# Performance work log

Measured on AMD Instinct MI355X. Metric: run time of the kernel, lower is better.

## Reference

```python
import jax, jax.numpy as jnp
import numpy as np

MAX_CONTEXT = 100
NUM_HEADS = 4
GRU_GROUPS = 4


def _layernorm(x, g, b, eps=1e-5):
    m = jnp.mean(x, axis=-1, keepdims=True)
    v = jnp.mean((x - m) ** 2, axis=-1, keepdims=True)
    return (x - m) / jnp.sqrt(v + eps) * g + b


def _grouped_gru(x, wih, whh, bih, bhh, G):
    # x: [N, T, C]; shared GRU params run on each channel group (PyTorch gate order r,z,n)
    N, T, C = x.shape
    D = C // G
    xg = x.reshape(N, T, G, D)
    xp = jnp.einsum('ntgd,ed->ntge', xg, wih) + bih  # e = 3D, precomputed input projections
    xp = jnp.moveaxis(xp, 1, 0)  # [T, N, G, 3D]

    def step(h, xt):
        gh = jnp.einsum('ngd,ed->nge', h, whh) + bhh
        xr, xz, xn = jnp.split(xt, 3, axis=-1)
        hr, hz, hn = jnp.split(gh, 3, axis=-1)
        r = jax.nn.sigmoid(xr + hr)
        z = jax.nn.sigmoid(xz + hz)
        n = jnp.tanh(xn + r * hn)
        h = (1.0 - z) * n + z * h
        return h, h

    h0 = jnp.zeros((N, G, D), x.dtype)
    _, hs = jax.lax.scan(step, h0, xp)  # hs: [T, N, G, D]
    return jnp.moveaxis(hs, 0, 1).reshape(N, T, C)


def _mha(x, wqkv, bqkv, wo, bo, H, max_ctx):
    # batch_first self-attention with causal + truncated-window additive mask
    N, T, C = x.shape
    Dh = C // H
    qkv = x @ wqkv.T + bqkv
    q, k, v = jnp.split(qkv, 3, axis=-1)
    q = q.reshape(N, T, H, Dh)
    k = k.reshape(N, T, H, Dh)
    v = v.reshape(N, T, H, Dh)
    scale = 1.0 / np.sqrt(Dh).astype(np.float32)
    scores = jnp.einsum('nqhd,nkhd->nhqk', q, k) * scale
    i = jnp.arange(T)
    diff = i[:, None] - i[None, :]
    allowed = (diff >= 0) & (diff <= max_ctx)
    scores = jnp.where(allowed, scores, -jnp.inf)
    attn = jax.nn.softmax(scores, axis=-1)
    out = jnp.einsum('nhqk,nkhd->nqhd', attn, v).reshape(N, T, C)
    return out @ wo.T + bo


def setup_inputs() -> dict:
    key = jax.random.key(0)
    ks = jax.random.split(key, 5)
    B, C, T, F = 2, 128, 512, 64
    D = C // GRU_GROUPS
    s = 0.1
    return {
        'x': jax.random.normal(ks[0], (B, C, T, F), jnp.float32),
        'ln1_g': jnp.ones((C,), jnp.float32),
        'ln1_b': jnp.zeros((C,), jnp.float32),
        'gru_wih': jax.random.normal(ks[1], (3 * D, D), jnp.float32) * s,
        'gru_whh': jax.random.normal(ks[2], (3 * D, D), jnp.float32) * s,
        'gru_bih': jnp.zeros((3 * D,), jnp.float32),
        'gru_bhh': jnp.zeros((3 * D,), jnp.float32),
        'ln2_g': jnp.ones((C,), jnp.float32),
        'ln2_b': jnp.zeros((C,), jnp.float32),
        'in_proj_w': jax.random.normal(ks[3], (3 * C, C), jnp.float32) * s,
        'in_proj_b': jnp.zeros((3 * C,), jnp.float32),
        'out_proj_w': jax.random.normal(ks[4], (C, C), jnp.float32) * s,
        'out_proj_b': jnp.zeros((C,), jnp.float32),
    }


def reference(x, ln1_g, ln1_b, gru_wih, gru_whh, gru_bih, gru_bhh, ln2_g, ln2_b, in_proj_w, in_proj_b, out_proj_w, out_proj_b):
    B, C, T, F = x.shape
    # [B, C, T, F] -> [B*F, T, C]: each freq bin is an independent time sequence
    seq = jnp.transpose(x, (0, 3, 2, 1)).reshape(B * F, T, C)
    seq = seq + _grouped_gru(_layernorm(seq, ln1_g, ln1_b), gru_wih, gru_whh, gru_bih, gru_bhh, GRU_GROUPS)
    seq = seq + _mha(_layernorm(seq, ln2_g, ln2_b), in_proj_w, in_proj_b, out_proj_w, out_proj_b, NUM_HEADS, MAX_CONTEXT)
    return jnp.transpose(seq.reshape(B, F, T, C), (0, 3, 2, 1))
```

## Files before the change

kernel.cpp:

```cpp
#include <hip/hip_runtime.h>
#include <hip/hip_bf16.h>
#include <math.h>


typedef __attribute__((ext_vector_type(8))) short short8;
typedef __attribute__((ext_vector_type(4))) float f32x4;
typedef __attribute__((ext_vector_type(2))) float f32x2;

__device__ __forceinline__ float bflo(unsigned int u) { return __uint_as_float(u << 16); }
__device__ __forceinline__ float bfhi(unsigned int u) { return __uint_as_float(u & 0xffff0000u); }
__device__ __forceinline__ float bf2f(unsigned short u) { return __uint_as_float(((unsigned int)u) << 16); }
__device__ __forceinline__ unsigned short f2bf(float f) {
  __hip_bfloat16 h = __float2bfloat16(f);
  return *reinterpret_cast<unsigned short*>(&h);
}

typedef __attribute__((address_space(1))) const unsigned int uint_g;
typedef __attribute__((address_space(3))) unsigned int uint_l;
__device__ __forceinline__ void glds16(const void* g, void* l) {
  __builtin_amdgcn_global_load_lds((uint_g*)g, (uint_l*)l, 16, 0, 0);
}

__global__ __launch_bounds__(256) void transpose_in_ln_kernel(const float* __restrict__ x,
                                                              float* __restrict__ seq,
                                                              const float* __restrict__ gam,
                                                              const float* __restrict__ bet,
                                                              unsigned short* __restrict__ out,
                                                              const float* __restrict__ wih,
                                                              unsigned short* __restrict__ wih_b,
                                                              const float* __restrict__ inw,
                                                              unsigned short* __restrict__ inw_b,
                                                              const float* __restrict__ outw,
                                                              unsigned short* __restrict__ outw_b) {
  {
    int g_ = blockIdx.x * 256 + threadIdx.x;
    if (g_ < 3072) wih_b[g_] = f2bf(wih[g_]);
    else if (g_ < 52224) inw_b[g_ - 3072] = f2bf(inw[g_ - 3072]);
    else if (g_ < 68608) outw_b[g_ - 52224] = f2bf(outw[g_ - 52224]);
  }

  __shared__ float tile[128 * 65];
  int b = blockIdx.x >> 9;
  int t = blockIdx.x & 511;
  for (int i = threadIdx.x; i < 128 * 64; i += 256) {
    int c = i >> 6, f = i & 63;
    tile[c * 65 + f] = x[(((size_t)(b * 128 + c)) * 512 + t) * 64 + f];
  }
  __syncthreads();
  for (int i = threadIdx.x; i < 64 * 128; i += 256) {
    int f = i >> 7, c = i & 127;
    seq[(((size_t)(b * 64 + f)) * 512 + t) * 128 + c] = tile[c * 65 + f];
  }

  const int f = threadIdx.x >> 2, q = threadIdx.x & 3;
  float s = 0.f, ss = 0.f;
  #pragma unroll
  for (int u = 0; u < 32; ++u) {
    float v = tile[(q * 32 + u) * 65 + f];
    s += v; ss += v * v;
  }
  s += __shfl_xor(s, 1); s += __shfl_xor(s, 2);
  ss += __shfl_xor(ss, 1); ss += __shfl_xor(ss, 2);
  float mean = s * (1.f / 128.f);
  float var = ss * (1.f / 128.f) - mean * mean;
  float rs = rsqrtf(var + 1e-5f);

  unsigned int* orow = (unsigned int*)(out + (((size_t)(b * 64 + f)) * 512 + t) * 128);
  #pragma unroll
  for (int u = 0; u < 8; ++u) {
    int c0 = q * 32 + u * 4;
    float4 gg = ((const float4*)gam)[c0 >> 2];
    float4 bb = ((const float4*)bet)[c0 >> 2];
    float v0 = tile[(c0 + 0) * 65 + f], v1 = tile[(c0 + 1) * 65 + f];
    float v2 = tile[(c0 + 2) * 65 + f], v3 = tile[(c0 + 3) * 65 + f];
    float o0 = (v0 - mean) * rs * gg.x + bb.x;
    float o1 = (v1 - mean) * rs * gg.y + bb.y;
    float o2 = (v2 - mean) * rs * gg.z + bb.z;
    float o3 = (v3 - mean) * rs * gg.w + bb.w;
    orow[(c0 >> 1) + 0] = ((unsigned int)f2bf(o1) << 16) | (unsigned int)f2bf(o0);
    orow[(c0 >> 1) + 1] = ((unsigned int)f2bf(o3) << 16) | (unsigned int)f2bf(o2);
  }
}

__global__ __launch_bounds__(256) void transpose_out_kernel(const float* __restrict__ seq, float* __restrict__ out) {
  __shared__ float tile[128 * 65];
  int b = blockIdx.x >> 9;
  int t = blockIdx.x & 511;
  for (int i = threadIdx.x; i < 64 * 128; i += 256) {
    int f = i >> 7, c = i & 127;
    tile[c * 65 + f] = seq[(((size_t)(b * 64 + f)) * 512 + t) * 128 + c];
  }
  __syncthreads();
  for (int i = threadIdx.x; i < 128 * 64; i += 256) {
    int c = i >> 6, f = i & 63;
    out[(((size_t)(b * 128 + c)) * 512 + t) * 64 + f] = tile[c * 65 + f];
  }
}

__global__ __launch_bounds__(256) void ln_kernel(const float* __restrict__ in, const float* __restrict__ g,
                                                 const float* __restrict__ b, unsigned short* __restrict__ out) {
  int row = blockIdx.x * 4 + (threadIdx.x >> 6);
  int lane = threadIdx.x & 63;
  float2 v = ((const float2*)(in + (size_t)row * 128))[lane];
  float s = v.x + v.y, ss = v.x * v.x + v.y * v.y;
  #pragma unroll
  for (int off = 32; off > 0; off >>= 1) {
    s += __shfl_xor(s, off);
    ss += __shfl_xor(ss, off);
  }
  float mean = s * (1.f / 128.f);
  float var = ss * (1.f / 128.f) - mean * mean;
  float rs = rsqrtf(var + 1e-5f);
  float2 gg = ((const float2*)g)[lane];
  float2 bb = ((const float2*)b)[lane];
  float o0 = (v.x - mean) * rs * gg.x + bb.x;
  float o1 = (v.y - mean) * rs * gg.y + bb.y;
  unsigned int packed = ((unsigned int)f2bf(o1) << 16) | (unsigned int)f2bf(o0);
  ((unsigned int*)(out + (size_t)row * 128))[lane] = packed;
}

template <int K, int MODE>
__global__ __launch_bounds__(256) void gemm_mfma(const unsigned short* __restrict__ A,
                                                 const unsigned short* __restrict__ W,
                                                 const float* __restrict__ bias,
                                                 unsigned short* __restrict__ outB,
                                                 float* __restrict__ outF, int Ncols) {
  const int tid = threadIdx.x;
  const int wave = tid >> 6, lane = tid & 63;
  const int wy = wave >> 1, wx = wave & 1;
  const int lr = lane & 15, lq = lane >> 4;
  const int m0 = blockIdx.x * 128 + wy * 64;
  const int n0 = blockIdx.y * 128 + wx * 64;

  f32x4 acc[4][4];
  #pragma unroll
  for (int i = 0; i < 4; ++i)
    #pragma unroll
    for (int j = 0; j < 4; ++j) acc[i][j] = f32x4{0.f, 0.f, 0.f, 0.f};

  const short8 zfrag = short8{0, 0, 0, 0, 0, 0, 0, 0};

  #pragma unroll
  for (int kk = 0; kk < K; kk += 32) {
    short8 af[4], bfq[4];
    #pragma unroll
    for (int i = 0; i < 4; ++i)
      af[i] = *(const short8*)(A + (size_t)(m0 + i * 16 + lr) * K + kk + lq * 8);
    #pragma unroll
    for (int j = 0; j < 4; ++j) {
      int wr = n0 + j * 16 + lr;
      bfq[j] = (wr < Ncols) ? *(const short8*)(W + (size_t)wr * K + kk + lq * 8) : zfrag;
    }
    #pragma unroll
    for (int i = 0; i < 4; ++i)
      #pragma unroll
      for (int j = 0; j < 4; ++j)
        acc[i][j] = __builtin_amdgcn_mfma_f32_16x16x32_bf16(af[i], bfq[j], acc[i][j], 0, 0, 0);
  }

  #pragma unroll
  for (int j = 0; j < 4; ++j) {
    int col = n0 + j * 16 + lr;
    if (col < Ncols) {
      float bb = bias[col];
      #pragma unroll
      for (int i = 0; i < 4; ++i) {
        #pragma unroll
        for (int r = 0; r < 4; ++r) {
          int row = m0 + i * 16 + lq * 4 + r;
          float v = acc[i][j][r] + bb;
          if (MODE == 0)
            outB[(size_t)row * Ncols + col] = f2bf(v);
          else
            outF[(size_t)row * 128 + col] += v;
        }
      }
    }
  }
}

__global__ __launch_bounds__(64, 1) void gru_kernel(const unsigned short* __restrict__ xp,
                                                    const float* __restrict__ whh,
                                                    const float* __restrict__ bhh,
                                                    float* __restrict__ seq) {
  const int l = threadIdx.x;
  const int half = l >> 5, d = l & 31;
  const int blk = blockIdx.x;
  const int chain = blk * 2 + half;
  const int n = chain >> 2;
  const int g0 = (blk * 2) & 3;

  const float LOG2E = 1.4426950408889634f;
  const float T2LOG2E = 2.8853900817779268f;

  __shared__ __align__(16) unsigned char stage[2][6144];
  __shared__ __align__(16) float h_lds[2][64];
  h_lds[0][l] = 0.f;

  f32x2 wr2[16], wz2[16], wn2[16];
  #pragma unroll
  for (int u = 0; u < 16; ++u) {
    float2 a = *(const float2*)(whh + (size_t)d * 32 + u * 2);
    float2 b = *(const float2*)(whh + (size_t)(32 + d) * 32 + u * 2);
    float2 c = *(const float2*)(whh + (size_t)(64 + d) * 32 + u * 2);
    wr2[u] = f32x2{a.x * LOG2E, a.y * LOG2E};
    wz2[u] = f32x2{b.x * LOG2E, b.y * LOG2E};
    wn2[u] = f32x2{c.x * T2LOG2E, c.y * T2LOG2E};
  }
  #pragma unroll
  for (int u = 0; u < 16; ++u)
    asm volatile("" : "+v"(wr2[u]), "+v"(wz2[u]), "+v"(wn2[u]));

  float br = bhh[d] * LOG2E, bz = bhh[32 + d] * LOG2E, bn = bhh[64 + d] * T2LOG2E;
  asm volatile("" : "+v"(br), "+v"(bz), "+v"(bn));

  const char* xg = (const char*)xp;
  const size_t cb0 = ((size_t)n * 2048 + g0) * 192;
  const size_t cb1 = ((size_t)n * 2048 + g0 + 1) * 192;
  const int fa = l * 16;
  const int oxa = (fa / 192) * 768 + (fa % 192);
  const int fb = 1024 + l * 16;
  const int oxb = (fb / 192) * 768 + (fb % 192);
  const char* px0a = xg + cb0 + oxa;
  const char* px0b = xg + cb0 + oxb;
  const char* px1a = xg + cb1 + oxa;
  const char* px1b = xg + cb1 + oxb;
  const int osa = (l >> 4) * 512 + (l & 15) * 16;
  const size_t sqb0 = ((size_t)n * 512 * 128 + (size_t)g0 * 32) * 4;
  const char* psa = (const char*)seq + sqb0 + osa;
  const char* psb = psa + 2048;

  float* sb = seq + (size_t)n * 512 * 128 + g0 * 32 + l;

  glds16(px0a, stage[0] + 0);
  glds16(px0b, stage[0] + 1024);
  glds16(px1a, stage[0] + 2048);
  glds16(px1b, stage[0] + 3072);
  glds16(psa,  stage[0] + 4096);
  glds16(psb,  stage[0] + 5120);

  float hprev = 0.f;

  for (int c = 0; c < 64; ++c) {
    const int cur = c & 1;
    if (c < 63) {
      const size_t xo = (size_t)(c + 1) * 6144;
      const size_t so = (size_t)(c + 1) * 4096;
      unsigned char* nb = stage[cur ^ 1];
      glds16(px0a + xo, nb + 0);
      glds16(px0b + xo, nb + 1024);
      glds16(px1a + xo, nb + 2048);
      glds16(px1b + xo, nb + 3072);
      glds16(psa + so,  nb + 4096);
      glds16(psb + so,  nb + 5120);
    }
    __builtin_amdgcn_sched_barrier(0);
    if (c == 0)       asm volatile("s_waitcnt vmcnt(6)" ::: "memory");
    else if (c == 63) asm volatile("s_waitcnt vmcnt(8)" ::: "memory");
    else              asm volatile("s_waitcnt vmcnt(14)" ::: "memory");
    __builtin_amdgcn_sched_barrier(0);

    const unsigned char* scur = stage[cur];
    #pragma unroll
    for (int p = 0; p < 8; ++p) {
      const int t = c * 8 + p;

      const f32x4* hsrc = (const f32x4*)&h_lds[p & 1][half * 32];
      f32x2 ar0 = f32x2{br, 0.f}, ar1 = f32x2{0.f, 0.f};
      f32x2 az0 = f32x2{bz, 0.f}, az1 = f32x2{0.f, 0.f};
      f32x2 an0 = f32x2{bn, 0.f}, an1 = f32x2{0.f, 0.f};
      #pragma unroll
      for (int u = 0; u < 8; ++u) {
        f32x4 h4 = hsrc[u];
        f32x2 hlo = f32x2{h4.x, h4.y};
        f32x2 hhi = f32x2{h4.z, h4.w};
        ar0 += wr2[2 * u] * hlo; ar1 += wr2[2 * u + 1] * hhi;
        az0 += wz2[2 * u] * hlo; az1 += wz2[2 * u + 1] * hhi;
        an0 += wn2[2 * u] * hlo; an1 += wn2[2 * u + 1] * hhi;
      }
      f32x2 arv = ar0 + ar1, azv = az0 + az1, anv = an0 + an1;
      float accr = arv.x + arv.y;
      float accz = azv.x + azv.y;
      float accn = anv.x + anv.y;

      const unsigned short* xrow = (const unsigned short*)(scur + half * 2048 + p * 192);
      float xr = bf2f(xrow[d]) * LOG2E;
      float xz = bf2f(xrow[32 + d]) * LOG2E;
      float xn2 = bf2f(xrow[64 + d]) * T2LOG2E;
      float sv0 = *(const float*)(scur + 4096 + p * 256 + (l << 2));

      float r = __builtin_amdgcn_rcpf(1.f + __builtin_amdgcn_exp2f(-(xr + accr)));
      float z = __builtin_amdgcn_rcpf(1.f + __builtin_amdgcn_exp2f(-(xz + accz)));
      float e2 = __builtin_amdgcn_exp2f(xn2 + r * accn);
      float nn = 1.f - 2.f * __builtin_amdgcn_rcpf(e2 + 1.f);
      float hnew = z * (hprev - nn) + nn;
      hprev = hnew;

      h_lds[(p + 1) & 1][l] = hnew;
      sb[(size_t)t * 128] = sv0 + hnew;
    }
  }
}

__global__ __launch_bounds__(256) void attn_oproj_kernel(const unsigned short* __restrict__ qkv,
                                                         const unsigned short* __restrict__ outw_b,
                                                         const float* __restrict__ outb,
                                                         float* __restrict__ seq) {
  const int qbase = blockIdx.x * 64;
  const int n = blockIdx.y;
  const int tid = threadIdx.x;
  const int w = tid >> 6, lane = tid & 63;
  const int lr = lane & 15, lq = lane >> 4;
  const int ws0 = max(0, qbase - 100);

  const int KROWS = 192;
  const int VPITCH = 200;
  const int PPITCH = 40;
  const int OPITCH = 132;

  __shared__ unsigned short KL[192 * 32];
  __shared__ unsigned short VT[32 * 200];
  __shared__ unsigned short PL[4][16 * 40];
  __shared__ float LL[64];
  __shared__ unsigned short OT[64 * 132];

  const char* qkvb = (const char*)qkv;
  const size_t rowb = ((size_t)(n * 512 + ws0)) * 768;
  const int wq0 = qbase + w * 16;

  const float SCL2 = 0.17677669529663687f * 1.4426950408889634f;
  const int lo = max(0, wq0 - 100) - ws0;
  const int hi = wq0 + 15 - ws0;
  const int kc0 = lo >> 5, kc1 = hi >> 5;
  unsigned short* plw = PL[w];

  for (int h = 0; h < 4; ++h) {
    if (h) __syncthreads();

    #pragma unroll
    for (int it = 0; it < 3; ++it) {
      int c = w * 192 + it * 64 + lane;
      const char* src = qkvb + rowb + (size_t)(c >> 2) * 768 + 256 + h * 64 + (size_t)(c & 3) * 16;
      glds16(src, (char*)KL + w * 3072 + it * 1024);
    }
    if (tid < KROWS) {
      const unsigned int* vsrc = (const unsigned int*)(qkvb + rowb + (size_t)tid * 768 + 512 + h * 64);
      #pragma unroll
      for (int u = 0; u < 16; ++u) {
        unsigned int vv = vsrc[u];
        VT[(2 * u) * VPITCH + tid] = (unsigned short)(vv & 0xffff);
        VT[(2 * u + 1) * VPITCH + tid] = (unsigned short)(vv >> 16);
      }
    }
    short8 qfrag = *(const short8*)(qkvb + ((size_t)(n * 512 + wq0 + lr)) * 768 + h * 64 + lq * 16);
    __syncthreads();

    f32x4 oacc0 = f32x4{0.f, 0.f, 0.f, 0.f};
    f32x4 oacc1 = f32x4{0.f, 0.f, 0.f, 0.f};
    float lsum[4] = {0.f, 0.f, 0.f, 0.f};

    for (int kc = kc0; kc <= kc1; ++kc) {
      #pragma unroll
      for (int sub = 0; sub < 2; ++sub) {
        const int kt = kc * 2 + sub;
        short8 kfrag = *(const short8*)(KL + (kt * 16 + lr) * 32 + lq * 8);
        f32x4 s4 = __builtin_amdgcn_mfma_f32_16x16x32_bf16(qfrag, kfrag,
                                                           f32x4{0.f, 0.f, 0.f, 0.f}, 0, 0, 0);
        const int tk = ws0 + kt * 16 + lr;
        #pragma unroll
        for (int r = 0; r < 4; ++r) {
          const int tq = wq0 + lq * 4 + r;
          bool ok = (tk <= tq) && (tk + 100 >= tq);
          float p = ok ? __builtin_amdgcn_exp2f(s4[r] * SCL2) : 0.f;
          lsum[r] += p;
          plw[(lq * 4 + r) * PPITCH + sub * 16 + lr] = f2bf(p);
        }
      }
      short8 pfrag = *(const short8*)(plw + lr * PPITCH + lq * 8);
      short8 vf0 = *(const short8*)(VT + lr * VPITCH + kc * 32 + lq * 8);
      short8 vf1 = *(const short8*)(VT + (16 + lr) * VPITCH + kc * 32 + lq * 8);
      oacc0 = __builtin_amdgcn_mfma_f32_16x16x32_bf16(vf0, pfrag, oacc0, 0, 0, 0);
      oacc1 = __builtin_amdgcn_mfma_f32_16x16x32_bf16(vf1, pfrag, oacc1, 0, 0, 0);
    }

    #pragma unroll
    for (int r = 0; r < 4; ++r) {
      float v = lsum[r];
      v += __shfl_xor(v, 1); v += __shfl_xor(v, 2);
      v += __shfl_xor(v, 4); v += __shfl_xor(v, 8);
      lsum[r] = v;
    }
    if (lr == 0) {
      #pragma unroll
      for (int r = 0; r < 4; ++r) LL[w * 16 + lq * 4 + r] = lsum[r];
    }
    float rl = __builtin_amdgcn_rcpf(LL[w * 16 + lr]);

    {
      unsigned short* orow = OT + (w * 16 + lr) * OPITCH + h * 32 + lq * 4;
      uint2 pk0;
      pk0.x = ((unsigned int)f2bf(oacc0[1] * rl) << 16) | f2bf(oacc0[0] * rl);
      pk0.y = ((unsigned int)f2bf(oacc0[3] * rl) << 16) | f2bf(oacc0[2] * rl);
      *(uint2*)orow = pk0;
      uint2 pk1;
      pk1.x = ((unsigned int)f2bf(oacc1[1] * rl) << 16) | f2bf(oacc1[0] * rl);
      pk1.y = ((unsigned int)f2bf(oacc1[3] * rl) << 16) | f2bf(oacc1[2] * rl);
      *(uint2*)(orow + 16) = pk1;
    }
  }

  __syncthreads();

  f32x4 acc[8];
  #pragma unroll
  for (int j = 0; j < 8; ++j) acc[j] = f32x4{0.f, 0.f, 0.f, 0.f};
  #pragma unroll
  for (int kk = 0; kk < 4; ++kk) {
    short8 af = *(const short8*)(OT + (w * 16 + lr) * OPITCH + kk * 32 + lq * 8);
    #pragma unroll
    for (int j = 0; j < 8; ++j) {
      short8 wf = *(const short8*)(outw_b + (size_t)(j * 16 + lr) * 128 + kk * 32 + lq * 8);
      acc[j] = __builtin_amdgcn_mfma_f32_16x16x32_bf16(af, wf, acc[j], 0, 0, 0);
    }
  }
  #pragma unroll
  for (int j = 0; j < 8; ++j) {
    int col = j * 16 + lr;
    float bb = outb[col];
    #pragma unroll
    for (int r = 0; r < 4; ++r) {
      size_t row = (size_t)n * 512 + qbase + w * 16 + lq * 4 + r;
      seq[row * 128 + col] += acc[j][r] + bb;
    }
  }
}

extern "C" void kernel_launch(void* const* d_in, const int* in_sizes, int n_in,
                              void* d_out, int out_size, void* d_ws, size_t ws_size,
                              hipStream_t stream) {
  const float* x      = (const float*)d_in[0];
  const float* ln1_g  = (const float*)d_in[1];
  const float* ln1_b  = (const float*)d_in[2];
  const float* wih    = (const float*)d_in[3];
  const float* whh    = (const float*)d_in[4];
  const float* bih    = (const float*)d_in[5];
  const float* bhh    = (const float*)d_in[6];
  const float* ln2_g  = (const float*)d_in[7];
  const float* ln2_b  = (const float*)d_in[8];
  const float* inw    = (const float*)d_in[9];
  const float* inb    = (const float*)d_in[10];
  const float* outw   = (const float*)d_in[11];
  const float* outb   = (const float*)d_in[12];

  char* ws = (char*)d_ws;
  float*          seq   = (float*)ws;
  unsigned short* tmpb  = (unsigned short*)(ws + 33554432);
  unsigned short* big   = (unsigned short*)(ws + 50331648);
  unsigned short* wih_b = (unsigned short*)(ws + 100663296);
  unsigned short* inw_b = wih_b + 3072;
  unsigned short* outw_b = inw_b + 49152;

  transpose_in_ln_kernel<<<1024, 256, 0, stream>>>(x, seq, ln1_g, ln1_b, tmpb,
                                                   wih, wih_b, inw, inw_b, outw, outw_b);

  gemm_mfma<32, 0><<<dim3(2048, 1), 256, 0, stream>>>(tmpb, wih_b, bih, big, nullptr, 96);

  gru_kernel<<<256, 64, 0, stream>>>(big, whh, bhh, seq);

  ln_kernel<<<16384, 256, 0, stream>>>(seq, ln2_g, ln2_b, tmpb);

  gemm_mfma<128, 0><<<dim3(512, 3), 256, 0, stream>>>(tmpb, inw_b, inb, big, nullptr, 384);

  attn_oproj_kernel<<<dim3(8, 128), 256, 0, stream>>>(big, outw_b, outb, seq);

  transpose_out_kernel<<<1024, 256, 0, stream>>>(seq, (float*)d_out);
}
```

Baseline: 382.9 us.

## Split attention per head across blocks and fuse output projection into transpose-out

The attention kernel now launches one block per (query tile, head, sequence) rather than looping over four heads inside a block, which gives four times as many blocks and lighter per-block work. It writes the bf16 attention output to a scratch buffer. The output projection and residual add move into the final transpose kernel, which computes them with MFMA and adds them to the LDS tile before the transposed store, removing a separate read-modify-write of seq. In exchange, the attention output makes an extra global round trip, and each head's block reloads its own K/V slices.

```diff
diff --git a/kernel.cpp b/kernel.cpp
--- a/kernel.cpp
+++ b/kernel.cpp
@@ -82,16 +82,51 @@
   }
 }
 
-__global__ __launch_bounds__(256) void transpose_out_kernel(const float* __restrict__ seq, float* __restrict__ out) {
+__global__ __launch_bounds__(256) void transpose_out_oproj_kernel(const float* __restrict__ seq,
+                                                                  const unsigned short* __restrict__ attn,
+                                                                  const unsigned short* __restrict__ outw_b,
+                                                                  const float* __restrict__ outb,
+                                                                  float* __restrict__ out) {
   __shared__ float tile[128 * 65];
   int b = blockIdx.x >> 9;
   int t = blockIdx.x & 511;
-  for (int i = threadIdx.x; i < 64 * 128; i += 256) {
+  const int tid = threadIdx.x;
+  const int w = tid >> 6, lane = tid & 63;
+  const int lr = lane & 15, lq = lane >> 4;
+
+  for (int i = tid; i < 64 * 128; i += 256) {
     int f = i >> 7, c = i & 127;
     tile[c * 65 + f] = seq[(((size_t)(b * 64 + f)) * 512 + t) * 128 + c];
   }
+
+  f32x4 acc[8];
+  #pragma unroll
+  for (int j = 0; j < 8; ++j) acc[j] = f32x4{0.f, 0.f, 0.f, 0.f};
+  const unsigned short* arow = attn + (((size_t)(b * 64 + w * 16 + lr)) * 512 + t) * 128;
+  #pragma unroll
+  for (int kk = 0; kk < 4; ++kk) {
+    short8 af = *(const short8*)(arow + kk * 32 + lq * 8);
+    #pragma unroll
+    for (int j = 0; j < 8; ++j) {
+      short8 wf = *(const short8*)(outw_b + (size_t)(j * 16 + lr) * 128 + kk * 32 + lq * 8);
+      acc[j] = __builtin_amdgcn_mfma_f32_16x16x32_bf16(af, wf, acc[j], 0, 0, 0);
+    }
+  }
   __syncthreads();
-  for (int i = threadIdx.x; i < 128 * 64; i += 256) {
+
+  #pragma unroll
+  for (int j = 0; j < 8; ++j) {
+    int col = j * 16 + lr;
+    float bb = outb[col];
+    #pragma unroll
+    for (int r = 0; r < 4; ++r) {
+      int f = w * 16 + lq * 4 + r;
+      tile[col * 65 + f] += acc[j][r] + bb;
+    }
+  }
+  __syncthreads();
+
+  for (int i = tid; i < 128 * 64; i += 256) {
     int c = i >> 6, f = i & 63;
     out[(((size_t)(b * 128 + c)) * 512 + t) * 64 + f] = tile[c * 65 + f];
   }
@@ -302,12 +337,11 @@
   }
 }
 
-__global__ __launch_bounds__(256) void attn_oproj_kernel(const unsigned short* __restrict__ qkv,
-                                                         const unsigned short* __restrict__ outw_b,
-                                                         const float* __restrict__ outb,
-                                                         float* __restrict__ seq) {
+__global__ __launch_bounds__(256) void attn_kernel(const unsigned short* __restrict__ qkv,
+                                                   unsigned short* __restrict__ outp) {
   const int qbase = blockIdx.x * 64;
-  const int n = blockIdx.y;
+  const int h = blockIdx.y;
+  const int n = blockIdx.z;
   const int tid = threadIdx.x;
   const int w = tid >> 6, lane = tid & 63;
   const int lr = lane & 15, lq = lane >> 4;
@@ -316,122 +350,93 @@
   const int KROWS = 192;
   const int VPITCH = 200;
   const int PPITCH = 40;
-  const int OPITCH = 132;
 
   __shared__ unsigned short KL[192 * 32];
   __shared__ unsigned short VT[32 * 200];
   __shared__ unsigned short PL[4][16 * 40];
   __shared__ float LL[64];
-  __shared__ unsigned short OT[64 * 132];
 
   const char* qkvb = (const char*)qkv;
   const size_t rowb = ((size_t)(n * 512 + ws0)) * 768;
+
   const int wq0 = qbase + w * 16;
+  short8 qfrag = *(const short8*)(qkvb + ((size_t)(n * 512 + wq0 + lr)) * 768 + h * 64 + lq * 16);
+
+  #pragma unroll
+  for (int it = 0; it < 3; ++it) {
+    int c = w * 192 + it * 64 + lane;
+    const char* src = qkvb + rowb + (size_t)(c >> 2) * 768 + 256 + h * 64 + (size_t)(c & 3) * 16;
+    glds16(src, (char*)KL + w * 3072 + it * 1024);
+  }
+
+  if (tid < KROWS) {
+    const unsigned int* vsrc = (const unsigned int*)(qkvb + rowb + (size_t)tid * 768 + 512 + h * 64);
+    #pragma unroll
+    for (int u = 0; u < 16; ++u) {
+      unsigned int vv = vsrc[u];
+      VT[(2 * u) * VPITCH + tid] = (unsigned short)(vv & 0xffff);
+      VT[(2 * u + 1) * VPITCH + tid] = (unsigned short)(vv >> 16);
+    }
+  }
+  __syncthreads();
 
   const float SCL2 = 0.17677669529663687f * 1.4426950408889634f;
   const int lo = max(0, wq0 - 100) - ws0;
   const int hi = wq0 + 15 - ws0;
   const int kc0 = lo >> 5, kc1 = hi >> 5;
+
+  f32x4 oacc0 = f32x4{0.f, 0.f, 0.f, 0.f};
+  f32x4 oacc1 = f32x4{0.f, 0.f, 0.f, 0.f};
+  float lsum[4] = {0.f, 0.f, 0.f, 0.f};
   unsigned short* plw = PL[w];
 
-  for (int h = 0; h < 4; ++h) {
-    if (h) __syncthreads();
-
-    #pragma unroll
-    for (int it = 0; it < 3; ++it) {
-      int c = w * 192 + it * 64 + lane;
-      const char* src = qkvb + rowb + (size_t)(c >> 2) * 768 + 256 + h * 64 + (size_t)(c & 3) * 16;
-      glds16(src, (char*)KL + w * 3072 + it * 1024);
-    }
-    if (tid < KROWS) {
-      const unsigned int* vsrc = (const unsigned int*)(qkvb + rowb + (size_t)tid * 768 + 512 + h * 64);
+  for (int kc = kc0; kc <= kc1; ++kc) {
+    #pragma unroll
+    for (int sub = 0; sub < 2; ++sub) {
+      const int kt = kc * 2 + sub;
+      short8 kfrag = *(const short8*)(KL + (kt * 16 + lr) * 32 + lq * 8);
+      f32x4 s4 = __builtin_amdgcn_mfma_f32_16x16x32_bf16(qfrag, kfrag,
+                                                         f32x4{0.f, 0.f, 0.f, 0.f}, 0, 0, 0);
+      const int tk = ws0 + kt * 16 + lr;
       #pragma unroll
-      for (int u = 0; u < 16; ++u) {
-        unsigned int vv = vsrc[u];
-        VT[(2 * u) * VPITCH + tid] = (unsigned short)(vv & 0xffff);
-        VT[(2 * u + 1) * VPITCH + tid] = (unsigned short)(vv >> 16);
+      for (int r = 0; r < 4; ++r) {
+        const int tq = wq0 + lq * 4 + r;
+        bool ok = (tk <= tq) && (tk + 100 >= tq);
+        float p = ok ? __builtin_amdgcn_exp2f(s4[r] * SCL2) : 0.f;
+        lsum[r] += p;
+        plw[(lq * 4 + r) * PPITCH + sub * 16 + lr] = f2bf(p);
       }
     }
-    short8 qfrag = *(const short8*)(qkvb + ((size_t)(n * 512 + wq0 + lr)) * 768 + h * 64 + lq * 16);
-    __syncthreads();
-
-    f32x4 oacc0 = f32x4{0.f, 0.f, 0.f, 0.f};
-    f32x4 oacc1 = f32x4{0.f, 0.f, 0.f, 0.f};
-    float lsum[4] = {0.f, 0.f, 0.f, 0.f};
-
-    for (int kc = kc0; kc <= kc1; ++kc) {
-      #pragma unroll
-      for (int sub = 0; sub < 2; ++sub) {
-        const int kt = kc * 2 + sub;
-        short8 kfrag = *(const short8*)(KL + (kt * 16 + lr) * 32 + lq * 8);
-        f32x4 s4 = __builtin_amdgcn_mfma_f32_16x16x32_bf16(qfrag, kfrag,
-                                                           f32x4{0.f, 0.f, 0.f, 0.f}, 0, 0, 0);
-        const int tk = ws0 + kt * 16 + lr;
-        #pragma unroll
-        for (int r = 0; r < 4; ++r) {
-          const int tq = wq0 + lq * 4 + r;
-          bool ok = (tk <= tq) && (tk + 100 >= tq);
-          float p = ok ? __builtin_amdgcn_exp2f(s4[r] * SCL2) : 0.f;
-          lsum[r] += p;
-          plw[(lq * 4 + r) * PPITCH + sub * 16 + lr] = f2bf(p);
-        }
-      }
-      short8 pfrag = *(const short8*)(plw + lr * PPITCH + lq * 8);
-      short8 vf0 = *(const short8*)(VT + lr * VPITCH + kc * 32 + lq * 8);
-      short8 vf1 = *(const short8*)(VT + (16 + lr) * VPITCH + kc * 32 + lq * 8);
-      oacc0 = __builtin_amdgcn_mfma_f32_16x16x32_bf16(vf0, pfrag, oacc0, 0, 0, 0);
-      oacc1 = __builtin_amdgcn_mfma_f32_16x16x32_bf16(vf1, pfrag, oacc1, 0, 0, 0);
-    }
-
-    #pragma unroll
-    for (int r = 0; r < 4; ++r) {
-      float v = lsum[r];
-      v += __shfl_xor(v, 1); v += __shfl_xor(v, 2);
-      v += __shfl_xor(v, 4); v += __shfl_xor(v, 8);
-      lsum[r] = v;
-    }
-    if (lr == 0) {
-      #pragma unroll
-      for (int r = 0; r < 4; ++r) LL[w * 16 + lq * 4 + r] = lsum[r];
-    }
-    float rl = __builtin_amdgcn_rcpf(LL[w * 16 + lr]);
-
-    {
-      unsigned short* orow = OT + (w * 16 + lr) * OPITCH + h * 32 + lq * 4;
-      uint2 pk0;
-      pk0.x = ((unsigned int)f2bf(oacc0[1] * rl) << 16) | f2bf(oacc0[0] * rl);
-      pk0.y = ((unsigned int)f2bf(oacc0[3] * rl) << 16) | f2bf(oacc0[2] * rl);
-      *(uint2*)orow = pk0;
-      uint2 pk1;
-      pk1.x = ((unsigned int)f2bf(oacc1[1] * rl) << 16) | f2bf(oacc1[0] * rl);
-      pk1.y = ((unsigned int)f2bf(oacc1[3] * rl) << 16) | f2bf(oacc1[2] * rl);
-      *(uint2*)(orow + 16) = pk1;
-    }
-  }
-
-  __syncthreads();
-
-  f32x4 acc[8];
-  #pragma unroll
-  for (int j = 0; j < 8; ++j) acc[j] = f32x4{0.f, 0.f, 0.f, 0.f};
-  #pragma unroll
-  for (int kk = 0; kk < 4; ++kk) {
-    short8 af = *(const short8*)(OT + (w * 16 + lr) * OPITCH + kk * 32 + lq * 8);
-    #pragma unroll
-    for (int j = 0; j < 8; ++j) {
-      short8 wf = *(const short8*)(outw_b + (size_t)(j * 16 + lr) * 128 + kk * 32 + lq * 8);
-      acc[j] = __builtin_amdgcn_mfma_f32_16x16x32_bf16(af, wf, acc[j], 0, 0, 0);
-    }
-  }
-  #pragma unroll
-  for (int j = 0; j < 8; ++j) {
-    int col = j * 16 + lr;
-    float bb = outb[col];
-    #pragma unroll
-    for (int r = 0; r < 4; ++r) {
-      size_t row = (size_t)n * 512 + qbase + w * 16 + lq * 4 + r;
-      seq[row * 128 + col] += acc[j][r] + bb;
-    }
+    short8 pfrag = *(const short8*)(plw + lr * PPITCH + lq * 8);
+    short8 vf0 = *(const short8*)(VT + lr * VPITCH + kc * 32 + lq * 8);
+    short8 vf1 = *(const short8*)(VT + (16 + lr) * VPITCH + kc * 32 + lq * 8);
+    oacc0 = __builtin_amdgcn_mfma_f32_16x16x32_bf16(vf0, pfrag, oacc0, 0, 0, 0);
+    oacc1 = __builtin_amdgcn_mfma_f32_16x16x32_bf16(vf1, pfrag, oacc1, 0, 0, 0);
+  }
+
+  #pragma unroll
+  for (int r = 0; r < 4; ++r) {
+    float v = lsum[r];
+    v += __shfl_xor(v, 1); v += __shfl_xor(v, 2);
+    v += __shfl_xor(v, 4); v += __shfl_xor(v, 8);
+    lsum[r] = v;
+  }
+  if (lr == 0) {
+    #pragma unroll
+    for (int r = 0; r < 4; ++r) LL[w * 16 + lq * 4 + r] = lsum[r];
+  }
+  float rl = __builtin_amdgcn_rcpf(LL[w * 16 + lr]);
+
+  unsigned short* ob = outp + ((size_t)(n * 512 + wq0 + lr)) * 128 + h * 32 + lq * 4;
+  {
+    unsigned int w0 = ((unsigned int)f2bf(oacc0[1] * rl) << 16) | f2bf(oacc0[0] * rl);
+    unsigned int w1 = ((unsigned int)f2bf(oacc0[3] * rl) << 16) | f2bf(oacc0[2] * rl);
+    uint2 pk0; pk0.x = w0; pk0.y = w1;
+    *(uint2*)ob = pk0;
+    unsigned int w2 = ((unsigned int)f2bf(oacc1[1] * rl) << 16) | f2bf(oacc1[0] * rl);
+    unsigned int w3 = ((unsigned int)f2bf(oacc1[3] * rl) << 16) | f2bf(oacc1[2] * rl);
+    uint2 pk1; pk1.x = w2; pk1.y = w3;
+    *(uint2*)(ob + 16) = pk1;
   }
 }
 
@@ -471,7 +476,7 @@
 
   gemm_mfma<128, 0><<<dim3(512, 3), 256, 0, stream>>>(tmpb, inw_b, inb, big, nullptr, 384);
 
-  attn_oproj_kernel<<<dim3(8, 128), 256, 0, stream>>>(big, outw_b, outb, seq);
-
-  transpose_out_kernel<<<1024, 256, 0, stream>>>(seq, (float*)d_out);
-}
+  attn_kernel<<<dim3(8, 4, 128), 256, 0, stream>>>(big, tmpb);
+
+  transpose_out_oproj_kernel<<<1024, 256, 0, stream>>>(seq, tmpb, outw_b, outb, (float*)d_out);
+}
```

Measured after the change: 353.3 us. 7.7% less time.
